# Performance work log

Hardware: AMD Instinct MI355X
Metric: run time of the kernel (lower is better)

The kernel has to match this reference:

```python
import jax, jax.numpy as jnp
import numpy as np
import math

B, S, D, H = 2, 2048, 1024, 16
DH = D // H

def setup_inputs() -> dict:
    key = jax.random.key(0)
    ks = jax.random.split(key, 12)
    s = 1.0 / math.sqrt(D)
    return {
        "q": jax.random.normal(ks[0], (B, S, D), jnp.float32),
        "k": jax.random.normal(ks[1], (B, S, D), jnp.float32),
        "v": jax.random.normal(ks[2], (B, S, D), jnp.float32),
        "mask": jnp.tril(jnp.ones((S, S), dtype=bool)),  # causal mask
        "Wq": jax.random.normal(ks[3], (D, D), jnp.float32) * s,
        "bq": jnp.zeros((D,), jnp.float32),
        "Wk": jax.random.normal(ks[4], (D, D), jnp.float32) * s,
        "bk": jnp.zeros((D,), jnp.float32),
        "Wv": jax.random.normal(ks[5], (D, D), jnp.float32) * s,
        "bv": jnp.zeros((D,), jnp.float32),
        "Wo": jax.random.normal(ks[6], (D, D), jnp.float32) * s,
        "bo": jnp.zeros((D,), jnp.float32),
    }

def _split_heads(x):
    b, s, _ = x.shape
    return x.reshape(b, s, H, DH).transpose(0, 2, 1, 3)  # [B,H,S,DH]

def reference(q, k, v, mask, Wq, bq, Wk, bk, Wv, bv, Wo, bo):
    qh = _split_heads(q @ Wq.T + bq)
    kh = _split_heads(k @ Wk.T + bk)
    vh = _split_heads(v @ Wv.T + bv)
    scale = 1.0 / math.sqrt(DH)
    scores = jnp.einsum('bhqd,bhkd->bhqk', qh, kh) * scale  # [B,H,S,S]
    scores = jnp.where(mask[None, None, :, :], scores, -jnp.inf)
    attn = jax.nn.softmax(scores, axis=-1)
    out = jnp.einsum('bhqk,bhkd->bhqd', attn, vh)  # [B,H,S,DH]
    out = out.transpose(0, 2, 1, 3).reshape(B, S, D)  # combine heads
    return out @ Wo.T + bo
```

## Files before the change

kernel.cpp:

```cpp
#include <hip/hip_runtime.h>

typedef unsigned int u32;
typedef unsigned short u16;
typedef __attribute__((ext_vector_type(8))) short bf16x8;
typedef __attribute__((ext_vector_type(8))) u16 u16x8;
typedef __attribute__((ext_vector_type(4))) u16 u16x4;
typedef __attribute__((ext_vector_type(4))) float f32x4;
typedef __attribute__((ext_vector_type(2))) u32 u32x2;

#define AS1 __attribute__((address_space(1)))
#define AS3 __attribute__((address_space(3)))

__device__ __forceinline__ void gload_lds16(const void* g, void* l) {
  __builtin_amdgcn_global_load_lds((const AS1 u32*)g, (AS3 u32*)l, 16, 0, 0);
}

__device__ __forceinline__ u16 f2bf(float f) {
  union { float f; u32 u; } x; x.f = f;
  u32 u = x.u;
  return (u16)((u + 0x7fffu + ((u >> 16) & 1u)) >> 16);
}

__device__ __forceinline__ u32 cvt_pk_bf16(float lo, float hi) {
  u32 r;
  asm("v_cvt_pk_bf16_f32 %0, %1, %2" : "=v"(r) : "v"(lo), "v"(hi));
  return r;
}

__device__ __forceinline__ float fexp2(float x) {
  float r;
  asm("v_exp_f32 %0, %1" : "=v"(r) : "v"(x));
  return r;
}

__global__ __launch_bounds__(256) void convert_w(
    const float* __restrict__ wq, const float* __restrict__ wk,
    const float* __restrict__ wv, const float* __restrict__ wo,
    u16* __restrict__ dst)
{
  int b = blockIdx.x, t = threadIdx.x;
  int w = b >> 9;
  const float* sp = (w == 0) ? wq : ((w == 1) ? wk : ((w == 2) ? wv : wo));
  size_t lb = (size_t)(b & 511) * 2048 + (size_t)t * 8;
  f32x4 f0 = *(const f32x4*)(sp + lb);
  f32x4 f1 = *(const f32x4*)(sp + lb + 4);
  u16x8 o;
  o[0]=f2bf(f0[0]); o[1]=f2bf(f0[1]); o[2]=f2bf(f0[2]); o[3]=f2bf(f0[3]);
  o[4]=f2bf(f1[0]); o[5]=f2bf(f1[1]); o[6]=f2bf(f1[2]); o[7]=f2bf(f1[3]);
  *(u16x8*)(dst + (size_t)b*2048 + (size_t)t*8) = o;
}

__global__ __launch_bounds__(256, 3) void gemm_qkv(
    const float* __restrict__ Xq, const float* __restrict__ Xk, const float* __restrict__ Xv,
    const u16* __restrict__ Wall,
    const float* __restrict__ bq, const float* __restrict__ bk, const float* __restrict__ bv,
    u16* __restrict__ Cqk, u16* __restrict__ VT)
{
  __shared__ __align__(16) u16 lds[24576];
  const int t = threadIdx.x;
  const int wid = t >> 6, l = t & 63;
  const int c = l & 15, g = l >> 4;
  const int u = blockIdx.x;
  const int lid = (u & 7) * 96 + (u >> 3);
  const int which = lid >> 8;
  const int r5 = lid & 255;
  const int m0 = (r5 >> 3) * 128, n0 = (r5 & 7) * 128;
  const float* Afp = (which == 0) ? Xq : ((which == 1) ? Xk : Xv);
  const u16* Bw = Wall + (size_t)which * 1048576;
  const int wr = wid >> 1, wc = wid & 1;

  const int srow = wid*16 + (l >> 2);
  const int schk = l & 3;
  const int aswz = ((schk ^ (srow & 3) ^ ((srow >> 2) & 3)) << 3);
  const float* Ag0 = Afp + (size_t)(m0 + srow)*1024      + schk*8;
  const float* Ag1 = Afp + (size_t)(m0 + 64 + srow)*1024 + schk*8;
  const int awr0 = srow*32 + aswz;
  const int awr1 = (srow + 64)*32 + aswz;
  const int sswz = aswz;
  const u16* Bsrc0 = Bw + (size_t)(n0 + srow)*1024      + sswz;
  const u16* Bsrc1 = Bw + (size_t)(n0 + 64 + srow)*1024 + sswz;
  const int wbase = wid * 512;

  f32x4 ra0, ra1, ra2, ra3;

#define A_LOAD(j) do { \
    const float* ap0_ = Ag0 + ((j) << 5); \
    const float* ap1_ = Ag1 + ((j) << 5); \
    ra0 = *(const f32x4*)ap0_; ra1 = *(const f32x4*)(ap0_ + 4); \
    ra2 = *(const f32x4*)ap1_; ra3 = *(const f32x4*)(ap1_ + 4); \
  } while (0)

#define A_CVT_WRITE(j) do { \
    const int bo_ = ((j) % 3) * 8192; \
    u16x8 w0_, w1_; u32* q0_ = (u32*)&w0_; u32* q1_ = (u32*)&w1_; \
    q0_[0]=cvt_pk_bf16(ra0[0],ra0[1]); q0_[1]=cvt_pk_bf16(ra0[2],ra0[3]); \
    q0_[2]=cvt_pk_bf16(ra1[0],ra1[1]); q0_[3]=cvt_pk_bf16(ra1[2],ra1[3]); \
    q1_[0]=cvt_pk_bf16(ra2[0],ra2[1]); q1_[1]=cvt_pk_bf16(ra2[2],ra2[3]); \
    q1_[2]=cvt_pk_bf16(ra3[0],ra3[1]); q1_[3]=cvt_pk_bf16(ra3[2],ra3[3]); \
    *(u16x8*)&lds[bo_ + awr0] = w0_; \
    *(u16x8*)&lds[bo_ + awr1] = w1_; \
  } while (0)

#define B_STAGE(j) do { \
    const int bo_ = ((j) % 3) * 8192; const int ko_ = (j) << 5; \
    gload_lds16(Bsrc0 + ko_, &lds[bo_ + 4096 + wbase]); \
    gload_lds16(Bsrc1 + ko_, &lds[bo_ + 6144 + wbase]); \
  } while (0)

  const int fswz = (g ^ (c & 3) ^ ((c >> 2) & 3)) << 3;
  const int abase = (wr*64 + c)*32 + fswz;
  const int bbase = 4096 + (wc*64 + c)*32 + fswz;

  f32x4 acc[4][4] = {};

  A_LOAD(0);
  B_STAGE(0);
  B_STAGE(1);
  asm volatile("s_waitcnt vmcnt(2)" ::: "memory");
  A_CVT_WRITE(0);
  A_LOAD(1);
  asm volatile("s_waitcnt lgkmcnt(0)" ::: "memory");
  __builtin_amdgcn_s_barrier();
  __builtin_amdgcn_sched_barrier(0);

#pragma unroll
  for (int tstep = 0; tstep < 32; ++tstep) {
    if (tstep + 2 < 32) B_STAGE(tstep + 2);
    const int bo = (tstep % 3) * 8192;
    bf16x8 af[4], bf[4];
#pragma unroll
    for (int mf = 0; mf < 4; ++mf)
      af[mf] = *(const bf16x8*)&lds[bo + abase + mf*512];
#pragma unroll
    for (int nf = 0; nf < 4; ++nf)
      bf[nf] = *(const bf16x8*)&lds[bo + bbase + nf*512];
    __builtin_amdgcn_s_setprio(1);
#pragma unroll
    for (int mf = 0; mf < 4; ++mf)
#pragma unroll
      for (int nf = 0; nf < 4; ++nf)
        acc[mf][nf] = __builtin_amdgcn_mfma_f32_16x16x32_bf16(af[mf], bf[nf], acc[mf][nf], 0, 0, 0);
    __builtin_amdgcn_s_setprio(0);
    if (tstep + 1 < 32) {
      if (tstep + 2 < 32) asm volatile("s_waitcnt vmcnt(2)" ::: "memory");
      else                asm volatile("s_waitcnt vmcnt(0)" ::: "memory");
      A_CVT_WRITE(tstep + 1);
      if (tstep + 2 < 32) A_LOAD(tstep + 2);
    }
    asm volatile("s_waitcnt lgkmcnt(0)" ::: "memory");
    __builtin_amdgcn_s_barrier();
    __builtin_amdgcn_sched_barrier(0);
  }
#undef A_LOAD
#undef A_CVT_WRITE
#undef B_STAGE

  const float* bias = (which == 0) ? bq : ((which == 1) ? bk : bv);
  if (which < 2) {
#pragma unroll
    for (int mf = 0; mf < 4; ++mf)
#pragma unroll
      for (int nf = 0; nf < 4; ++nf) {
        int row = m0 + wr*64 + mf*16 + g*4;
        int col = n0 + wc*64 + nf*16 + c;
        float bv_ = bias[col];
        int colg = which*1024 + col;
#pragma unroll
        for (int r = 0; r < 4; ++r)
          Cqk[(size_t)(row+r)*2048 + colg] = f2bf(acc[mf][nf][r] + bv_);
      }
  } else {
#pragma unroll
    for (int mf = 0; mf < 4; ++mf)
#pragma unroll
      for (int nf = 0; nf < 4; ++nf) {
        int row = m0 + wr*64 + mf*16 + g*4;
        int col = n0 + wc*64 + nf*16 + c;
        float bv_ = bias[col];
        int bb2 = row >> 11, s = row & 2047;
        int hh = col >> 6, dh = col & 63;
        u16x4 pk;
#pragma unroll
        for (int r = 0; r < 4; ++r) pk[r] = f2bf(acc[mf][nf][r] + bv_);
        *(u16x4*)&VT[((size_t)(((bb2<<4)+hh)<<6) + dh)*2048 + s] = pk;
      }
  }
}

__global__ __launch_bounds__(256, 3) void gemm_out(
    const u16* __restrict__ A, const u16* __restrict__ Bw,
    const float* __restrict__ bias, float* __restrict__ C)
{
  __shared__ __align__(16) u16 lds[24576];
  const int t = threadIdx.x;
  const int wid = t >> 6, l = t & 63;
  const int c = l & 15, g = l >> 4;
  const int u = blockIdx.x;
  const int lid = (u & 7) * 32 + (u >> 3);
  const int m0 = (lid >> 3) * 128, n0 = (lid & 7) * 128;
  const int wr = wid >> 1, wc = wid & 1;

  const int srow = wid*16 + (l >> 2);
  const int sswz = (((l & 3) ^ (srow & 3) ^ ((srow >> 2) & 3)) << 3);
  const u16* Asrc0 = A  + (size_t)(m0 + srow)*1024      + sswz;
  const u16* Asrc1 = A  + (size_t)(m0 + 64 + srow)*1024 + sswz;
  const u16* Bsrc0 = Bw + (size_t)(n0 + srow)*1024      + sswz;
  const u16* Bsrc1 = Bw + (size_t)(n0 + 64 + srow)*1024 + sswz;
  const int wbase = wid * 512;

#define O_STAGE(j) do { \
    const int bo_ = ((j) % 3) * 8192; const int ko_ = (j) << 5; \
    gload_lds16(Asrc0 + ko_, &lds[bo_ + wbase]); \
    gload_lds16(Asrc1 + ko_, &lds[bo_ + 2048 + wbase]); \
    gload_lds16(Bsrc0 + ko_, &lds[bo_ + 4096 + wbase]); \
    gload_lds16(Bsrc1 + ko_, &lds[bo_ + 6144 + wbase]); \
  } while (0)

  const int fswz = (g ^ (c & 3) ^ ((c >> 2) & 3)) << 3;
  const int abase = (wr*64 + c)*32 + fswz;
  const int bbase = 4096 + (wc*64 + c)*32 + fswz;

  f32x4 acc[4][4] = {};

  O_STAGE(0);
  O_STAGE(1);
  asm volatile("s_waitcnt vmcnt(4)" ::: "memory");
  __builtin_amdgcn_s_barrier();
  __builtin_amdgcn_sched_barrier(0);

#pragma unroll
  for (int tstep = 0; tstep < 32; ++tstep) {
    if (tstep + 2 < 32) O_STAGE(tstep + 2);
    const int bo = (tstep % 3) * 8192;
    bf16x8 af[4], bf[4];
#pragma unroll
    for (int mf = 0; mf < 4; ++mf)
      af[mf] = *(const bf16x8*)&lds[bo + abase + mf*512];
#pragma unroll
    for (int nf = 0; nf < 4; ++nf)
      bf[nf] = *(const bf16x8*)&lds[bo + bbase + nf*512];
    __builtin_amdgcn_s_setprio(1);
#pragma unroll
    for (int mf = 0; mf < 4; ++mf)
#pragma unroll
      for (int nf = 0; nf < 4; ++nf)
        acc[mf][nf] = __builtin_amdgcn_mfma_f32_16x16x32_bf16(af[mf], bf[nf], acc[mf][nf], 0, 0, 0);
    __builtin_amdgcn_s_setprio(0);
    if (tstep + 2 < 32) asm volatile("s_waitcnt vmcnt(4)" ::: "memory");
    else                asm volatile("s_waitcnt vmcnt(0)" ::: "memory");
    __builtin_amdgcn_s_barrier();
    __builtin_amdgcn_sched_barrier(0);
  }
#undef O_STAGE

#pragma unroll
  for (int mf = 0; mf < 4; ++mf)
#pragma unroll
    for (int nf = 0; nf < 4; ++nf) {
      int row = m0 + wr*64 + mf*16 + g*4;
      int col = n0 + wc*64 + nf*16 + c;
      float bv_ = bias[col];
#pragma unroll
      for (int r = 0; r < 4; ++r)
        C[(size_t)(row+r)*1024 + col] = acc[mf][nf][r] + bv_;
    }
}

__device__ __forceinline__ void stage_kv(u16* lds, const u16* Kt, const u16* Vt,
                                         int buf, int wid) {
#pragma unroll
  for (int ii = 0; ii < 2; ++ii)
    gload_lds16(Kt + (size_t)ii*32*2048, &lds[4096 + buf*4096 + ii*2048 + wid*512]);
#pragma unroll
  for (int ii = 0; ii < 2; ++ii)
    gload_lds16(Vt + (size_t)ii*32*2048, &lds[12288 + buf*4096 + ii*2048 + wid*512]);
}

__device__ __forceinline__ void attn_phase(
    u16* lds, const u16* Qg, const u16* Ka, const u16* Va,
    int q0, int kt0, int nkv, bool maskLast,
    int wid, int g, int c, int arow, int achk, int pbase, int cs,
    float& MI, float& LI, f32x4 (&o)[4])
{
  const float SC = 0.18033688f;
#pragma unroll
  for (int i = 0; i < 2; ++i) {
    int row = i*32 + arow;
    gload_lds16(Qg + (size_t)(q0+row)*2048 + ((achk ^ (row&7)) << 3),
                &lds[i*2048 + wid*512]);
  }
  const u16* Kt = Ka + (size_t)kt0 * (64*2048);
  const u16* Vt = Va + kt0 * 64;
  stage_kv(lds, Kt, Vt, 0, wid);
  asm volatile("s_waitcnt vmcnt(0)" ::: "memory");
  __builtin_amdgcn_s_barrier();
  __builtin_amdgcn_sched_barrier(0);

  bf16x8 qf[2];
#pragma unroll
  for (int kh = 0; kh < 2; ++kh) {
    int row = wid*16 + c;
    int ch = (kh*4 + g) ^ (row & 7);
    qf[kh] = *(const bf16x8*)&lds[row*64 + ch*8];
  }

  float mi = -INFINITY, li = 0.f;
#pragma unroll
  for (int df = 0; df < 4; ++df) o[df] = f32x4{0.f, 0.f, 0.f, 0.f};

  for (int i = 0; i < nkv; ++i) {
    if (i + 1 < nkv) {
      Kt += 64*2048; Vt += 64;
      stage_kv(lds, Kt, Vt, (i+1)&1, wid);
    }
    const u16* Kb = &lds[4096  + (i&1)*4096];
    const u16* Vb = &lds[12288 + (i&1)*4096];

    f32x4 sT[4] = {};
    __builtin_amdgcn_s_setprio(1);
#pragma unroll
    for (int kh = 0; kh < 2; ++kh) {
      bf16x8 kf[4];
#pragma unroll
      for (int nf = 0; nf < 4; ++nf) {
        int row = nf*16 + c;
        int ch = (kh*4 + g) ^ (c & 7);
        kf[nf] = *(const bf16x8*)&Kb[row*64 + ch*8];
      }
#pragma unroll
      for (int nf = 0; nf < 4; ++nf)
        sT[nf] = __builtin_amdgcn_mfma_f32_16x16x32_bf16(kf[nf], qf[kh], sT[nf], 0,0,0);
    }
    __builtin_amdgcn_s_setprio(0);

    if (maskLast && i == nkv - 1) {
#pragma unroll
      for (int nf = 0; nf < 4; ++nf)
#pragma unroll
        for (int r = 0; r < 4; ++r)
          if (nf*16 + g*4 + r > wid*16 + c) sT[nf][r] = -INFINITY;
    }

    float mx = fmaxf(fmaxf(sT[0][0], sT[0][1]), fmaxf(sT[0][2], sT[0][3]));
#pragma unroll
    for (int nf = 1; nf < 4; ++nf)
      mx = fmaxf(mx, fmaxf(fmaxf(sT[nf][0], sT[nf][1]), fmaxf(sT[nf][2], sT[nf][3])));
    if (!__all(mx * SC <= mi + 8.f)) {
      float mxr = fmaxf(mx, __shfl_xor(mx, 16, 64));
      mxr = fmaxf(mxr, __shfl_xor(mxr, 32, 64));
      float mn = fmaxf(mi, mxr * SC);
      float corr = fexp2(mi - mn);
      li *= corr;
#pragma unroll
      for (int df = 0; df < 4; ++df) {
        o[df][0] *= corr; o[df][1] *= corr;
        o[df][2] *= corr; o[df][3] *= corr;
      }
      mi = mn;
    }
    float sum = 0.f;
#pragma unroll
    for (int nf = 0; nf < 4; ++nf)
#pragma unroll
      for (int r = 0; r < 4; ++r) {
        float pv = fexp2(fmaf(sT[nf][r], SC, -mi));
        sT[nf][r] = pv;
        sum += pv;
      }
    li += sum;

#pragma unroll
    for (int nf = 0; nf < 4; ++nf) {
      u32x2 ww;
      ww[0] = cvt_pk_bf16(sT[nf][0], sT[nf][1]);
      ww[1] = cvt_pk_bf16(sT[nf][2], sT[nf][3]);
      int ch = (2*nf + (g >> 1)) ^ cs;
      *(u32x2*)&lds[pbase + c*64 + ch*8 + (g & 1)*4] = ww;
    }
    asm volatile("s_waitcnt lgkmcnt(0)" ::: "memory");
    __builtin_amdgcn_sched_barrier(0);

    __builtin_amdgcn_s_setprio(1);
#pragma unroll
    for (int kh = 0; kh < 2; ++kh) {
      bf16x8 pfr, vf[4];
      {
        int ch = (kh*4 + g) ^ cs;
        pfr = *(const bf16x8*)&lds[pbase + c*64 + ch*8];
      }
#pragma unroll
      for (int df = 0; df < 4; ++df) {
        int d = df*16 + c;
        int ch = (kh*4 + g) ^ (d & 7);
        vf[df] = *(const bf16x8*)&Vb[d*64 + ch*8];
      }
#pragma unroll
      for (int df = 0; df < 4; ++df)
        o[df] = __builtin_amdgcn_mfma_f32_16x16x32_bf16(vf[df], pfr, o[df], 0,0,0);
    }
    __builtin_amdgcn_s_setprio(0);

    asm volatile("s_waitcnt vmcnt(0)" ::: "memory");
    __builtin_amdgcn_s_barrier();
    __builtin_amdgcn_sched_barrier(0);
  }
  MI = mi; LI = li;
}

__device__ __forceinline__ void store_partial(
    float* __restrict__ part, int slot, int s,
    int wid, int g, int c, float mi, float li_tot, const f32x4 (&o)[4])
{
  float* po = part + (size_t)(slot*2 + s) * 4224;
  int q = wid*16 + c;
#pragma unroll
  for (int df = 0; df < 4; ++df)
    *(f32x4*)&po[q*64 + df*16 + g*4] = o[df];
  if (g == 0) { po[4096 + q] = mi; po[4160 + q] = li_tot; }
}

__global__ __launch_bounds__(256, 4) void attn_fwd(
    const u16* __restrict__ QK, const u16* __restrict__ VT,
    u16* __restrict__ AO, float* __restrict__ part)
{
  __shared__ __align__(16) u16 lds[20480];
  const int t = threadIdx.x;
  const int wid = t >> 6, l = t & 63;
  const int g = l >> 4, c = l & 15;
  const int u = blockIdx.x;
  const int lid = (u & 7) * 128 + (u >> 3);
  const int gx = lid & 31, h = (lid >> 5) & 15, b = lid >> 9;
  const int p = gx >> 1, s = gx & 1;
  const u16* Qg  = QK + (size_t)b * 2048 * 2048 + (size_t)h * 64;
  const u16* Kg  = Qg + 1024;
  const u16* VTg = VT + (size_t)(((b << 4) + h) << 6) * 2048;
  const int arow = t >> 3, achk = t & 7;
  const int pbase = wid * 1024;
  const int cs = (c & 7) ^ ((c >> 3) << 2);
  const u16* Ka = Kg  + (size_t)arow*2048 + ((achk ^ (arow & 7)) << 3);
  const u16* Va = VTg + (size_t)arow*2048 + ((achk ^ (arow & 7)) << 3);
  const int slot = ((b*16 + h)*16 + p);

  float mi, li; f32x4 o[4];

  if (s == 0) {
    attn_phase(lds, Qg, Ka, Va, p*64, 0, p+1, true,
               wid, g, c, arow, achk, pbase, cs, mi, li, o);
    {
      float lt = li + __shfl_xor(li, 16, 64);
      lt += __shfl_xor(lt, 32, 64);
      float nr = 1.f / lt;
      int row = p*64 + wid*16 + c;
      size_t rb = ((size_t)b*2048 + row)*1024 + h*64;
#pragma unroll
      for (int df = 0; df < 4; ++df) {
        u16x4 pk;
        pk[0] = f2bf(o[df][0] * nr); pk[1] = f2bf(o[df][1] * nr);
        pk[2] = f2bf(o[df][2] * nr); pk[3] = f2bf(o[df][3] * nr);
        *(u16x4*)&AO[rb + df*16 + g*4] = pk;
      }
    }
    attn_phase(lds, Qg, Ka, Va, (31-p)*64, 0, 16-p, false,
               wid, g, c, arow, achk, pbase, cs, mi, li, o);
    float lt = li + __shfl_xor(li, 16, 64);
    lt += __shfl_xor(lt, 32, 64);
    store_partial(part, slot, 0, wid, g, c, mi, lt, o);
  } else {
    attn_phase(lds, Qg, Ka, Va, (31-p)*64, 16-p, 16, true,
               wid, g, c, arow, achk, pbase, cs, mi, li, o);
    float lt = li + __shfl_xor(li, 16, 64);
    lt += __shfl_xor(lt, 32, 64);
    store_partial(part, slot, 1, wid, g, c, mi, lt, o);
  }
}

__global__ __launch_bounds__(256) void attn_merge(
    const float* __restrict__ part, u16* __restrict__ AO)
{
  int slot = blockIdx.x;
  int p = slot & 15;
  int h = (slot >> 4) & 15;
  int b = slot >> 8;
  const float* p0 = part + (size_t)slot * 8448;
  const float* p1 = p0 + 4224;
  int t = threadIdx.x;
  int r = t >> 2, c0 = (t & 3) * 16;
  float m0 = p0[4096 + r], m1 = p1[4096 + r];
  float l0 = p0[4160 + r], l1 = p1[4160 + r];
  float m = fmaxf(m0, m1);
  float e0 = exp2f(m0 - m), e1 = exp2f(m1 - m);
  float rl = 1.f / (l0*e0 + l1*e1);
  e0 *= rl; e1 *= rl;
  const f32x4* a0 = (const f32x4*)(p0 + r*64 + c0);
  const f32x4* a1 = (const f32x4*)(p1 + r*64 + c0);
  u16x8 w0, w1;
#pragma unroll
  for (int q4 = 0; q4 < 4; ++q4) {
    f32x4 x = a0[q4], y = a1[q4];
#pragma unroll
    for (int j = 0; j < 4; ++j) {
      u16 bf = f2bf(x[j]*e0 + y[j]*e1);
      if (q4 < 2) w0[q4*4+j] = bf; else w1[(q4-2)*4+j] = bf;
    }
  }
  int qrow = (31 - p)*64 + r;
  size_t ab = ((size_t)b*2048 + qrow)*1024 + h*64 + c0;
  *(u16x8*)&AO[ab]     = w0;
  *(u16x8*)&AO[ab + 8] = w1;
}

extern "C" void kernel_launch(void* const* d_in, const int* in_sizes, int n_in,
                              void* d_out, int out_size, void* d_ws, size_t ws_size,
                              hipStream_t stream)
{
  const float* q  = (const float*)d_in[0];
  const float* k  = (const float*)d_in[1];
  const float* v  = (const float*)d_in[2];
  const float* Wq = (const float*)d_in[4];
  const float* bq = (const float*)d_in[5];
  const float* Wk = (const float*)d_in[6];
  const float* bk = (const float*)d_in[7];
  const float* Wv = (const float*)d_in[8];
  const float* bv = (const float*)d_in[9];
  const float* Wo = (const float*)d_in[10];
  const float* bo = (const float*)d_in[11];
  float* out = (float*)d_out;

  u16* ws   = (u16*)d_ws;
  u16* Wqb  = ws + 12582912;
  u16* Wob  = ws + 15728640;
  u16* QKp  = ws + 16777216;
  u16* VTp  = ws + 25165824;
  u16* AO   = ws + 29360128;

  convert_w<<<2048, 256, 0, stream>>>(Wq, Wk, Wv, Wo, Wqb);

  gemm_qkv<<<768, 256, 0, stream>>>(q, k, v, Wqb, bq, bk, bv, QKp, VTp);

  attn_fwd<<<1024, 256, 0, stream>>>(QKp, VTp, AO, (float*)d_ws);

  attn_merge<<<512, 256, 0, stream>>>((const float*)d_ws, AO);

  gemm_out<<<256, 256, 0, stream>>>(AO, Wob, bo, out);
}
```

Measured before the change: 101.8 us.

## Pre-convert q/k/v activations to bf16 and stream A tiles directly into LDS

The standalone weight-conversion kernel now also converts the q, k and v activations to bf16 into the workspace. The QKV GEMM then loads its A tiles with direct global-to-LDS loads, the same path B already uses, in place of fp32 register loads followed by in-kernel conversion and LDS writes. This simplifies the GEMM pipeline and halves the bytes it reads for A. In exchange it adds a separate pass that reads all fp32 activations and writes bf16 copies, which may cost more than the GEMM saves.

```diff
diff --git a/kernel.cpp b/kernel.cpp
--- a/kernel.cpp
+++ b/kernel.cpp
@@ -33,15 +33,23 @@
   return r;
 }
 
-__global__ __launch_bounds__(256) void convert_w(
+__global__ __launch_bounds__(256) void convert_all(
+    const float* __restrict__ q, const float* __restrict__ k, const float* __restrict__ v,
     const float* __restrict__ wq, const float* __restrict__ wk,
     const float* __restrict__ wv, const float* __restrict__ wo,
     u16* __restrict__ dst)
 {
   int b = blockIdx.x, t = threadIdx.x;
-  int w = b >> 9;
-  const float* sp = (w == 0) ? wq : ((w == 1) ? wk : ((w == 2) ? wv : wo));
-  size_t lb = (size_t)(b & 511) * 2048 + (size_t)t * 8;
+  const float* sp; size_t lb;
+  if (b < 6144) {
+    sp = (b < 2048) ? q : ((b < 4096) ? k : v);
+    lb = (size_t)(b & 2047) * 2048;
+  } else {
+    int w = (b - 6144) >> 9;
+    sp = (w == 0) ? wq : ((w == 1) ? wk : ((w == 2) ? wv : wo));
+    lb = (size_t)((b - 6144) & 511) * 2048;
+  }
+  lb += (size_t)t * 8;
   f32x4 f0 = *(const f32x4*)(sp + lb);
   f32x4 f1 = *(const f32x4*)(sp + lb + 4);
   u16x8 o;
@@ -51,7 +59,7 @@
 }
 
 __global__ __launch_bounds__(256, 3) void gemm_qkv(
-    const float* __restrict__ Xq, const float* __restrict__ Xk, const float* __restrict__ Xv,
+    const u16* __restrict__ Xall,
     const u16* __restrict__ Wall,
     const float* __restrict__ bq, const float* __restrict__ bk, const float* __restrict__ bv,
     u16* __restrict__ Cqk, u16* __restrict__ VT)
@@ -65,44 +73,22 @@
   const int which = lid >> 8;
   const int r5 = lid & 255;
   const int m0 = (r5 >> 3) * 128, n0 = (r5 & 7) * 128;
-  const float* Afp = (which == 0) ? Xq : ((which == 1) ? Xk : Xv);
+  const u16* A  = Xall + (size_t)which * 4194304;
   const u16* Bw = Wall + (size_t)which * 1048576;
   const int wr = wid >> 1, wc = wid & 1;
 
   const int srow = wid*16 + (l >> 2);
-  const int schk = l & 3;
-  const int aswz = ((schk ^ (srow & 3) ^ ((srow >> 2) & 3)) << 3);
-  const float* Ag0 = Afp + (size_t)(m0 + srow)*1024      + schk*8;
-  const float* Ag1 = Afp + (size_t)(m0 + 64 + srow)*1024 + schk*8;
-  const int awr0 = srow*32 + aswz;
-  const int awr1 = (srow + 64)*32 + aswz;
-  const int sswz = aswz;
+  const int sswz = ((l & 3) ^ (srow & 3) ^ ((srow >> 2) & 3)) << 3;
+  const u16* Asrc0 = A  + (size_t)(m0 + srow)*1024      + sswz;
+  const u16* Asrc1 = A  + (size_t)(m0 + 64 + srow)*1024 + sswz;
   const u16* Bsrc0 = Bw + (size_t)(n0 + srow)*1024      + sswz;
   const u16* Bsrc1 = Bw + (size_t)(n0 + 64 + srow)*1024 + sswz;
   const int wbase = wid * 512;
 
-  f32x4 ra0, ra1, ra2, ra3;
-
-#define A_LOAD(j) do { \
-    const float* ap0_ = Ag0 + ((j) << 5); \
-    const float* ap1_ = Ag1 + ((j) << 5); \
-    ra0 = *(const f32x4*)ap0_; ra1 = *(const f32x4*)(ap0_ + 4); \
-    ra2 = *(const f32x4*)ap1_; ra3 = *(const f32x4*)(ap1_ + 4); \
-  } while (0)
-
-#define A_CVT_WRITE(j) do { \
-    const int bo_ = ((j) % 3) * 8192; \
-    u16x8 w0_, w1_; u32* q0_ = (u32*)&w0_; u32* q1_ = (u32*)&w1_; \
-    q0_[0]=cvt_pk_bf16(ra0[0],ra0[1]); q0_[1]=cvt_pk_bf16(ra0[2],ra0[3]); \
-    q0_[2]=cvt_pk_bf16(ra1[0],ra1[1]); q0_[3]=cvt_pk_bf16(ra1[2],ra1[3]); \
-    q1_[0]=cvt_pk_bf16(ra2[0],ra2[1]); q1_[1]=cvt_pk_bf16(ra2[2],ra2[3]); \
-    q1_[2]=cvt_pk_bf16(ra3[0],ra3[1]); q1_[3]=cvt_pk_bf16(ra3[2],ra3[3]); \
-    *(u16x8*)&lds[bo_ + awr0] = w0_; \
-    *(u16x8*)&lds[bo_ + awr1] = w1_; \
-  } while (0)
-
-#define B_STAGE(j) do { \
+#define QKV_STAGE(j) do { \
     const int bo_ = ((j) % 3) * 8192; const int ko_ = (j) << 5; \
+    gload_lds16(Asrc0 + ko_, &lds[bo_ + wbase]); \
+    gload_lds16(Asrc1 + ko_, &lds[bo_ + 2048 + wbase]); \
     gload_lds16(Bsrc0 + ko_, &lds[bo_ + 4096 + wbase]); \
     gload_lds16(Bsrc1 + ko_, &lds[bo_ + 6144 + wbase]); \
   } while (0)
@@ -113,19 +99,15 @@
 
   f32x4 acc[4][4] = {};
 
-  A_LOAD(0);
-  B_STAGE(0);
-  B_STAGE(1);
-  asm volatile("s_waitcnt vmcnt(2)" ::: "memory");
-  A_CVT_WRITE(0);
-  A_LOAD(1);
-  asm volatile("s_waitcnt lgkmcnt(0)" ::: "memory");
+  QKV_STAGE(0);
+  QKV_STAGE(1);
+  asm volatile("s_waitcnt vmcnt(4)" ::: "memory");
   __builtin_amdgcn_s_barrier();
   __builtin_amdgcn_sched_barrier(0);
 
 #pragma unroll
   for (int tstep = 0; tstep < 32; ++tstep) {
-    if (tstep + 2 < 32) B_STAGE(tstep + 2);
+    if (tstep + 2 < 32) QKV_STAGE(tstep + 2);
     const int bo = (tstep % 3) * 8192;
     bf16x8 af[4], bf[4];
 #pragma unroll
@@ -141,19 +123,12 @@
       for (int nf = 0; nf < 4; ++nf)
         acc[mf][nf] = __builtin_amdgcn_mfma_f32_16x16x32_bf16(af[mf], bf[nf], acc[mf][nf], 0, 0, 0);
     __builtin_amdgcn_s_setprio(0);
-    if (tstep + 1 < 32) {
-      if (tstep + 2 < 32) asm volatile("s_waitcnt vmcnt(2)" ::: "memory");
-      else                asm volatile("s_waitcnt vmcnt(0)" ::: "memory");
-      A_CVT_WRITE(tstep + 1);
-      if (tstep + 2 < 32) A_LOAD(tstep + 2);
-    }
-    asm volatile("s_waitcnt lgkmcnt(0)" ::: "memory");
+    if (tstep + 2 < 32) asm volatile("s_waitcnt vmcnt(4)" ::: "memory");
+    else                asm volatile("s_waitcnt vmcnt(0)" ::: "memory");
     __builtin_amdgcn_s_barrier();
     __builtin_amdgcn_sched_barrier(0);
   }
-#undef A_LOAD
-#undef A_CVT_WRITE
-#undef B_STAGE
+#undef QKV_STAGE
 
   const float* bias = (which == 0) ? bq : ((which == 1) ? bk : bv);
   if (which < 2) {
@@ -527,15 +502,16 @@
   float* out = (float*)d_out;
 
   u16* ws   = (u16*)d_ws;
+  u16* qb   = ws;
   u16* Wqb  = ws + 12582912;
   u16* Wob  = ws + 15728640;
   u16* QKp  = ws + 16777216;
   u16* VTp  = ws + 25165824;
   u16* AO   = ws + 29360128;
 
-  convert_w<<<2048, 256, 0, stream>>>(Wq, Wk, Wv, Wo, Wqb);
-
-  gemm_qkv<<<768, 256, 0, stream>>>(q, k, v, Wqb, bq, bk, bv, QKp, VTp);
+  convert_all<<<8192, 256, 0, stream>>>(q, k, v, Wq, Wk, Wv, Wo, qb);
+
+  gemm_qkv<<<768, 256, 0, stream>>>(qb, Wqb, bq, bk, bv, QKp, VTp);
 
   attn_fwd<<<1024, 256, 0, stream>>>(QKp, VTp, AO, (float*)d_ws);
 
```

After: 106.4 us. 1.05x slower.
